# Kernel tuning notes

Measured on AMD Instinct MI355X. Metric: run time of the kernel, lower is better.

## Reference

```python
import jax, jax.numpy as jnp
import numpy as np

# Hyperparameters (match init_kwargs)
NOSHF_S = 64
NOSHF_R = 64
NOSHF_THETA = 64
LOWER_S, UPPER_S = -3.0, 3.0
LOWER_R, UPPER_R = -3.0, 3.0
LOWER_THETA, UPPER_THETA = 0.0, float(np.pi)
OETA_S = 8.0
OETA_R = 8.0
OZETA = 8.0
Z_TABLE = np.array([1, 6, 7, 8, 9, 16, 17])  # H C N O F S Cl -> rows 0..6
NCONF, NATOMS = 256, 128


def setup_inputs() -> dict:
    key = jax.random.key(0)
    k1, k2, k3, k4 = jax.random.split(key, 4)
    coefficients = jax.random.normal(k1, (NCONF, NATOMS, 21), dtype=jnp.float32)
    mus = jax.random.normal(k2, (2, 7, 9), dtype=jnp.float32) * 0.1
    sigmas = jax.random.uniform(k3, (2, 7, 9), dtype=jnp.float32, minval=0.5, maxval=1.5)
    # order: s_coeffs_mus, s_coeffs_sigmas, p_norms_mus, p_norms_sigmas
    normalization_library = jnp.stack([mus[0], sigmas[0], mus[1], sigmas[1]], axis=0)
    codes = jax.random.randint(k4, (NCONF, NATOMS), 0, 7)
    species = jnp.asarray(Z_TABLE, dtype=jnp.int64 if jax.config.jax_enable_x64 else jnp.int32)[codes]
    return {"coefficients": coefficients, "normalization_library": normalization_library, "species": species}


def reference(coefficients, normalization_library, species):
    nc, na, _ = coefficients.shape
    # species Z -> table row index
    z = jnp.asarray(Z_TABLE)
    sidx = jnp.argmax(species[..., None] == z, axis=-1)  # (nc, na)

    s_mus, s_sig, p_mus, p_sig = normalization_library
    p_mus = p_mus[:, :4]
    p_sig = p_sig[:, :4]

    # s-type coefficients: normalize then gaussian-shift expand
    s = coefficients[:, :, :9]
    s = (s - s_mus[sidx]) / s_sig[sidx]  # (nc, na, 9)
    shfS = jnp.linspace(LOWER_S, UPPER_S, NOSHF_S, dtype=jnp.float32)
    s_aev = jnp.exp(-OETA_S * (s[..., None] - shfS) ** 2).reshape(nc, na, 9 * NOSHF_S)

    # p-type: orbital matrix (nc, na, 4 AOVs, 3) -> norms, normalize, radial expand
    M = coefficients[:, :, 9:21].reshape(nc, na, 4, 3)
    p_norms = jnp.linalg.norm(M, axis=-1)  # (nc, na, 4)
    p_norms = (p_norms - p_mus[sidx]) / p_sig[sidx]
    shfR = jnp.linspace(LOWER_R, UPPER_R, NOSHF_R, dtype=jnp.float32)
    r_aev = jnp.exp(-OETA_R * (p_norms[..., None] - shfR) ** 2).reshape(nc, na, 4 * NOSHF_R)

    # angles between AOVs (rows normalized by the *normalized* norms, as in source)
    zero_mask = jnp.all(jnp.abs(M) < 1e-12, axis=-1)  # (nc, na, 4)
    Mn = jnp.where(zero_mask[..., None], 0.0, M / p_norms[..., None])
    G = jnp.einsum('bnik,bnjk->bnij', Mn, Mn)  # (nc, na, 4, 4)
    iu, ju = np.triu_indices(4, 1)  # 6 pairs, same row-major order as the loops
    cos_angles = jnp.clip(G[:, :, iu, ju], -0.9999, 0.9999)  # (nc, na, 6)
    angles = jnp.arccos(cos_angles)

    shfT = jnp.linspace(LOWER_THETA, UPPER_THETA, NOSHF_THETA, dtype=jnp.float32)
    ang = (2.0 ** (1.0 - OZETA)) * ((1.0 + jnp.cos(angles[..., None] - shfT)) / 2.0) ** OZETA
    ang_aev = ang.reshape(nc, na, 6 * NOSHF_THETA)

    return jnp.concatenate([s_aev, r_aev, ang_aev], axis=-1)  # (nc, na, 1216)
```

## Files before the change

### kernel.cpp

```cpp
#include <hip/hip_runtime.h>
#include <hip/hip_bf16.h>
#include <math.h>

#define NCONF  256
#define NATOMS 128
#define NATOT  (NCONF * NATOMS)
#define PER_ATOM 1216
#define NQUAD  304
#define TOTQ   (NATOT * NQUAD)
#define PSTR   25
#define WS_FLOATS (128 + NATOT * PSTR)

__device__ __forceinline__ int species_to_sidx(int z) {
    switch (z) {
        case 1:  return 0;
        case 6:  return 1;
        case 7:  return 2;
        case 8:  return 3;
        case 9:  return 4;
        case 16: return 5;
        default: return 6;
    }
}

__global__ __launch_bounds__(256) void aev_params_kernel(
    const float* __restrict__ coeff,
    const float* __restrict__ nlib,
    const int*   __restrict__ sp32,
    float* __restrict__ ws)
{
    const int tid  = threadIdx.x;
    const int atom = blockIdx.x * blockDim.x + tid;

    if (blockIdx.x == 0 && tid < 64) {
        float t = (float)tid * (float)(M_PI / 63.0);
        ws[tid]      = cosf(t);
        ws[64 + tid] = sinf(t);
    }
    if (atom >= NATOT) return;

    const int is64 = (sp32[1] == 0);
    const int z = is64 ? sp32[(size_t)atom * 2] : sp32[atom];
    const int sidx = species_to_sidx(z);

    const float* c     = coeff + (size_t)atom * 21;
    const float* s_mus = nlib + 0 * 63 + sidx * 9;
    const float* s_sig = nlib + 1 * 63 + sidx * 9;
    const float* p_mus = nlib + 2 * 63 + sidx * 9;
    const float* p_sig = nlib + 3 * 63 + sidx * 9;

    float* P = ws + 128 + (size_t)atom * PSTR;

    #pragma unroll
    for (int k = 0; k < 9; ++k)
        P[k] = (c[k] - s_mus[k]) / s_sig[k];

    float M[4][3];
    #pragma unroll
    for (int i = 0; i < 4; ++i) {
        M[i][0] = c[9 + i * 3 + 0];
        M[i][1] = c[9 + i * 3 + 1];
        M[i][2] = c[9 + i * 3 + 2];
        float nn  = M[i][0]*M[i][0] + M[i][1]*M[i][1] + M[i][2]*M[i][2];
        float nrm = sqrtf(nn);
        bool zero = (fabsf(M[i][0]) < 1e-12f) &&
                    (fabsf(M[i][1]) < 1e-12f) &&
                    (fabsf(M[i][2]) < 1e-12f);
        P[9 + i] = (nrm - p_mus[i]) / p_sig[i];
        float inv = zero ? 0.0f : (1.0f / nrm);
        M[i][0] *= inv; M[i][1] *= inv; M[i][2] *= inv;
    }
    const int iu[6] = {0, 0, 0, 1, 1, 2};
    const int ju[6] = {1, 2, 3, 2, 3, 3};
    #pragma unroll
    for (int p = 0; p < 6; ++p) {
        int i = iu[p], j = ju[p];
        float d = M[i][0]*M[j][0] + M[i][1]*M[j][1] + M[i][2]*M[j][2];
        d = fminf(fmaxf(d, -0.9999f), 0.9999f);
        P[13 + p] = d;
        P[19 + p] = sqrtf(fmaxf(1.0f - d * d, 0.0f));
    }
}

__global__ __launch_bounds__(256) void aev_stream_kernel(
    const float* __restrict__ ws,
    float* __restrict__ out)
{
    const int g = blockIdx.x * 256 + threadIdx.x;
    if (g >= TOTQ) return;
    const int atom = g / NQUAD;
    const int q    = g - atom * NQUAD;
    const int ch   = q >> 4;
    const int j0   = (q & 15) << 2;

    const float* P = ws + 128 + (size_t)atom * PSTR;
    const float K = 11.541560327111707f;

    float vv[4];
    if (ch < 13) {
        float x = P[ch];
        #pragma unroll
        for (int jj = 0; jj < 4; ++jj) {
            float shf = -3.0f + (float)(j0 + jj) * (6.0f / 63.0f);
            float d = x - shf;
            vv[jj] = exp2f(-K * d * d);
        }
    } else {
        int p = ch - 13;
        float cap = P[13 + p], sap = P[19 + p];
        float4 ct = *reinterpret_cast<const float4*>(ws + j0);
        float4 st = *reinterpret_cast<const float4*>(ws + 64 + j0);
        float cts[4] = {ct.x, ct.y, ct.z, ct.w};
        float sts[4] = {st.x, st.y, st.z, st.w};
        #pragma unroll
        for (int jj = 0; jj < 4; ++jj) {
            float t  = 0.5f + 0.5f * (cap * cts[jj] + sap * sts[jj]);
            float t2 = t * t;
            float t4 = t2 * t2;
            vv[jj] = 0.0078125f * (t4 * t4);
        }
    }
    float4 v; v.x = vv[0]; v.y = vv[1]; v.z = vv[2]; v.w = vv[3];
    *reinterpret_cast<float4*>(out + (size_t)atom * PER_ATOM + q * 4) = v;
}

__global__ __launch_bounds__(256) void aev_mono_kernel(
    const float* __restrict__ coeff,
    const float* __restrict__ nlib,
    const int*   __restrict__ sp32,
    float* __restrict__ out)
{
    __shared__ float s_chan[13];
    __shared__ float s_ca[6], s_sa[6];
    __shared__ float s_ct[64], s_st[64];

    const int atom = blockIdx.x;
    const int tid  = threadIdx.x;

    if (tid < 64) {
        float t = (float)tid * (float)(M_PI / 63.0);
        s_ct[tid] = cosf(t);
        s_st[tid] = sinf(t);
    }
    if (tid == 0) {
        const float* c = coeff + (size_t)atom * 21;
        const int is64 = (sp32[1] == 0);
        const int z = is64 ? sp32[(size_t)atom * 2] : sp32[atom];
        const int sidx = species_to_sidx(z);
        const float* s_mus = nlib + 0 * 63 + sidx * 9;
        const float* s_sig = nlib + 1 * 63 + sidx * 9;
        const float* p_mus = nlib + 2 * 63 + sidx * 9;
        const float* p_sig = nlib + 3 * 63 + sidx * 9;
        #pragma unroll
        for (int k = 0; k < 9; ++k)
            s_chan[k] = (c[k] - s_mus[k]) / s_sig[k];
        float M[4][3];
        #pragma unroll
        for (int i = 0; i < 4; ++i) {
            M[i][0] = c[9+i*3+0]; M[i][1] = c[9+i*3+1]; M[i][2] = c[9+i*3+2];
            float nn  = M[i][0]*M[i][0] + M[i][1]*M[i][1] + M[i][2]*M[i][2];
            float nrm = sqrtf(nn);
            bool zero = (fabsf(M[i][0]) < 1e-12f) && (fabsf(M[i][1]) < 1e-12f) &&
                        (fabsf(M[i][2]) < 1e-12f);
            s_chan[9+i] = (nrm - p_mus[i]) / p_sig[i];
            float inv = zero ? 0.0f : (1.0f / nrm);
            M[i][0] *= inv; M[i][1] *= inv; M[i][2] *= inv;
        }
        const int iu[6] = {0,0,0,1,1,2};
        const int ju[6] = {1,2,3,2,3,3};
        #pragma unroll
        for (int p = 0; p < 6; ++p) {
            int i = iu[p], j = ju[p];
            float d = M[i][0]*M[j][0] + M[i][1]*M[j][1] + M[i][2]*M[j][2];
            d = fminf(fmaxf(d, -0.9999f), 0.9999f);
            s_ca[p] = d;
            s_sa[p] = sqrtf(fmaxf(1.0f - d*d, 0.0f));
        }
    }
    __syncthreads();

    float* po = out + (size_t)atom * PER_ATOM;
    const float K = 11.541560327111707f;
    for (int q = tid; q < NQUAD; q += 256) {
        const int ch = q >> 4;
        const int j0 = (q & 15) << 2;
        float vv[4];
        if (ch < 13) {
            float x = s_chan[ch];
            #pragma unroll
            for (int jj = 0; jj < 4; ++jj) {
                float shf = -3.0f + (float)(j0 + jj) * (6.0f / 63.0f);
                float d = x - shf;
                vv[jj] = exp2f(-K * d * d);
            }
        } else {
            int p = ch - 13;
            float cap = s_ca[p], sap = s_sa[p];
            #pragma unroll
            for (int jj = 0; jj < 4; ++jj) {
                float t  = 0.5f + 0.5f * (cap * s_ct[j0+jj] + sap * s_st[j0+jj]);
                float t2 = t * t;
                float t4 = t2 * t2;
                vv[jj] = 0.0078125f * (t4 * t4);
            }
        }
        float4 v; v.x = vv[0]; v.y = vv[1]; v.z = vv[2]; v.w = vv[3];
        *reinterpret_cast<float4*>(po + q * 4) = v;
    }
}

extern "C" void kernel_launch(void* const* d_in, const int* in_sizes, int n_in,
                              void* d_out, int out_size, void* d_ws, size_t ws_size,
                              hipStream_t stream) {
    const float* coeff   = (const float*)d_in[0];
    const float* nlib    = (const float*)d_in[1];
    const int*   sp32    = (const int*)d_in[2];
    float* out           = (float*)d_out;
    float* ws            = (float*)d_ws;

    if (ws_size >= (size_t)WS_FLOATS * sizeof(float)) {
        aev_params_kernel<<<dim3((NATOT + 255) / 256), dim3(256), 0, stream>>>(
            coeff, nlib, sp32, ws);
        aev_stream_kernel<<<dim3(TOTQ / 256), dim3(256), 0, stream>>>(ws, out);
    } else {
        aev_mono_kernel<<<dim3(NATOT), dim3(256), 0, stream>>>(
            coeff, nlib, sp32, out);
    }
}
```

Before: 38.98 us.

## Transpose param workspace to SoA, fold constants, give each thread four output quads

The per-atom parameter workspace moves from an array-of-structs with stride 25 to a struct-of-arrays layout indexed by channel*NATOT, so that adjacent threads read adjacent addresses. The Gaussian scale sqrt(K) and the angular half-scale factor are folded into the stored parameters, which removes multiplies and the final constant scale in the streaming kernel. Each thread now writes 4 float4 quads strided by 76 instead of one, giving a quarter as many threads. The stores of one thread are spread out, so per-instruction store coalescing could change, and the folded constants could shift rounding slightly.

```diff
diff --git a/kernel.cpp b/kernel.cpp
--- a/kernel.cpp
+++ b/kernel.cpp
@@ -7,9 +7,15 @@
 #define NATOT  (NCONF * NATOMS)
 #define PER_ATOM 1216
 #define NQUAD  304
+#define QS     76
 #define TOTQ   (NATOT * NQUAD)
 #define PSTR   25
 #define WS_FLOATS (128 + NATOT * PSTR)
+
+#define SQK      3.3972871196167196f
+#define SK_STEP  0.32355115424921137f
+#define SK_BASE -10.191861358850159f
+#define HS       0.27262693316631437f
 
 __device__ __forceinline__ int species_to_sidx(int z) {
     switch (z) {
@@ -49,11 +55,11 @@
     const float* p_mus = nlib + 2 * 63 + sidx * 9;
     const float* p_sig = nlib + 3 * 63 + sidx * 9;
 
-    float* P = ws + 128 + (size_t)atom * PSTR;
+    float* P = ws + 128 + atom;
 
     #pragma unroll
     for (int k = 0; k < 9; ++k)
-        P[k] = (c[k] - s_mus[k]) / s_sig[k];
+        P[k * NATOT] = SQK * (c[k] - s_mus[k]) / s_sig[k];
 
     float M[4][3];
     #pragma unroll
@@ -66,7 +72,7 @@
         bool zero = (fabsf(M[i][0]) < 1e-12f) &&
                     (fabsf(M[i][1]) < 1e-12f) &&
                     (fabsf(M[i][2]) < 1e-12f);
-        P[9 + i] = (nrm - p_mus[i]) / p_sig[i];
+        P[(9 + i) * NATOT] = SQK * (nrm - p_mus[i]) / p_sig[i];
         float inv = zero ? 0.0f : (1.0f / nrm);
         M[i][0] *= inv; M[i][1] *= inv; M[i][2] *= inv;
     }
@@ -77,8 +83,9 @@
         int i = iu[p], j = ju[p];
         float d = M[i][0]*M[j][0] + M[i][1]*M[j][1] + M[i][2]*M[j][2];
         d = fminf(fmaxf(d, -0.9999f), 0.9999f);
-        P[13 + p] = d;
-        P[19 + p] = sqrtf(fmaxf(1.0f - d * d, 0.0f));
+        float sa = sqrtf(fmaxf(1.0f - d * d, 0.0f));
+        P[(13 + p) * NATOT] = HS * d;
+        P[(19 + p) * NATOT] = HS * sa;
     }
 }
 
@@ -87,41 +94,44 @@
     float* __restrict__ out)
 {
     const int g = blockIdx.x * 256 + threadIdx.x;
-    if (g >= TOTQ) return;
-    const int atom = g / NQUAD;
-    const int q    = g - atom * NQUAD;
-    const int ch   = q >> 4;
-    const int j0   = (q & 15) << 2;
-
-    const float* P = ws + 128 + (size_t)atom * PSTR;
-    const float K = 11.541560327111707f;
-
-    float vv[4];
-    if (ch < 13) {
-        float x = P[ch];
-        #pragma unroll
-        for (int jj = 0; jj < 4; ++jj) {
-            float shf = -3.0f + (float)(j0 + jj) * (6.0f / 63.0f);
-            float d = x - shf;
-            vv[jj] = exp2f(-K * d * d);
-        }
-    } else {
-        int p = ch - 13;
-        float cap = P[13 + p], sap = P[19 + p];
-        float4 ct = *reinterpret_cast<const float4*>(ws + j0);
-        float4 st = *reinterpret_cast<const float4*>(ws + 64 + j0);
-        float cts[4] = {ct.x, ct.y, ct.z, ct.w};
-        float sts[4] = {st.x, st.y, st.z, st.w};
-        #pragma unroll
-        for (int jj = 0; jj < 4; ++jj) {
-            float t  = 0.5f + 0.5f * (cap * cts[jj] + sap * sts[jj]);
-            float t2 = t * t;
-            float t4 = t2 * t2;
-            vv[jj] = 0.0078125f * (t4 * t4);
-        }
-    }
-    float4 v; v.x = vv[0]; v.y = vv[1]; v.z = vv[2]; v.w = vv[3];
-    *reinterpret_cast<float4*>(out + (size_t)atom * PER_ATOM + q * 4) = v;
+    const int atom = g / QS;
+    const int r    = g - atom * QS;
+
+    const float* P = ws + 128 + atom;
+    float* po = out + (size_t)atom * PER_ATOM;
+
+    #pragma unroll
+    for (int k = 0; k < 4; ++k) {
+        const int q  = r + k * QS;
+        const int ch = q >> 4;
+        const int j0 = (q & 15) << 2;
+        float vv[4];
+        if (ch < 13) {
+            const float X = P[ch * NATOT];
+            #pragma unroll
+            for (int jj = 0; jj < 4; ++jj) {
+                float d = X - fmaf((float)(j0 + jj), SK_STEP, SK_BASE);
+                vv[jj] = exp2f(-(d * d));
+            }
+        } else {
+            const int p = ch - 13;
+            const float A = P[(13 + p) * NATOT];
+            const float B = P[(19 + p) * NATOT];
+            const float4 ct = *reinterpret_cast<const float4*>(ws + j0);
+            const float4 st = *reinterpret_cast<const float4*>(ws + 64 + j0);
+            const float cts[4] = {ct.x, ct.y, ct.z, ct.w};
+            const float sts[4] = {st.x, st.y, st.z, st.w};
+            #pragma unroll
+            for (int jj = 0; jj < 4; ++jj) {
+                float u  = fmaf(A, cts[jj], fmaf(B, sts[jj], HS));
+                float u2 = u * u;
+                float u4 = u2 * u2;
+                vv[jj] = u4 * u4;
+            }
+        }
+        float4 v; v.x = vv[0]; v.y = vv[1]; v.z = vv[2]; v.w = vv[3];
+        *reinterpret_cast<float4*>(po + q * 4) = v;
+    }
 }
 
 __global__ __launch_bounds__(256) void aev_mono_kernel(
@@ -221,7 +231,7 @@
     if (ws_size >= (size_t)WS_FLOATS * sizeof(float)) {
         aev_params_kernel<<<dim3((NATOT + 255) / 256), dim3(256), 0, stream>>>(
             coeff, nlib, sp32, ws);
-        aev_stream_kernel<<<dim3(TOTQ / 256), dim3(256), 0, stream>>>(ws, out);
+        aev_stream_kernel<<<dim3((NATOT * QS) / 256), dim3(256), 0, stream>>>(ws, out);
     } else {
         aev_mono_kernel<<<dim3(NATOT), dim3(256), 0, stream>>>(
             coeff, nlib, sp32, out);
```

Result: slower. 40.46 us (+3.8%).
